# Performance work log

Measured on AMD Instinct MI355X. Metric: run time of the kernel, lower is better.

The kernel has to match this reference:

```python
import jax, jax.numpy as jnp
import numpy as np

N_IN = 1_000_000   # input mesh vertices
C = 128            # feature channels
N_OUT = 250_000


def setup_inputs() -> dict:
    key = jax.random.key(0)
    k1, k2, k3 = jax.random.split(key, 3)
    inputs = jax.random.normal(k1, (N_IN, C), dtype=jnp.float32)
    # cluster representative vertex for each input vertex
    vt_replace = jax.random.randint(k2, (N_IN,), 0, N_IN, dtype=jnp.int32)
    # output vertex id assigned to each (representative) vertex
    vt_map = jax.random.randint(k3, (N_IN,), 0, N_OUT, dtype=jnp.int32)
    return {"inputs": inputs, "vt_replace": vt_replace, "vt_map": vt_map, "vt_out": N_OUT}


def reference(inputs, vt_replace, vt_map, vt_out):
    # segment id of each input vertex: output slot of its cluster representative
    seg = vt_map[vt_replace]                     # [N_IN] int32 in [0, vt_out)
    # scatter-max reduce over irregular clusters -> [vt_out, C]
    out = jax.ops.segment_max(inputs, seg, num_segments=vt_out)
    # empty output vertices get 0 (segment_max fills with -inf)
    out = jnp.where(jnp.isfinite(out), out, jnp.zeros((), out.dtype))
    return out
```

## Files before the change

kernel.cpp:

```cpp
#include <hip/hip_runtime.h>
#include <stdint.h>

#define C_CH 128
#define SCAN_THREADS 256
#define SCAN_PER_THREAD 8
#define SCAN_ELEMS (SCAN_THREADS * SCAN_PER_THREAD)

typedef float floatx4 __attribute__((ext_vector_type(4)));

__device__ __forceinline__ unsigned fkey(float x) {
  unsigned b = __float_as_uint(x);
  return b ^ ((unsigned)((int)b >> 31) | 0x80000000u);
}
__device__ __forceinline__ float fdec(unsigned k) {
  unsigned b = (k & 0x80000000u) ? (k & 0x7FFFFFFFu) : ~k;
  return __uint_as_float(b);
}

__global__ __launch_bounds__(256) void pool_atomic(
    const float4* __restrict__ in4, const int* __restrict__ vt_replace,
    const int* __restrict__ vt_map, unsigned* __restrict__ outk, int64_t n4) {
  const int64_t stride = (int64_t)gridDim.x * blockDim.x;
  for (int64_t t = (int64_t)blockIdx.x * blockDim.x + threadIdx.x; t < n4;
       t += stride) {
    const int row = (int)(t >> 5);
    const int c4  = (int)(t & 31);
    int s = 0;
    if ((threadIdx.x & 31) == 0) s = vt_map[vt_replace[row]];
    s = __shfl(s, 0, 32);
    const float4 v = in4[t];
    unsigned* o = outk + ((int64_t)s << 7) + (c4 << 2);
    atomicMax(o + 0, fkey(v.x));
    atomicMax(o + 1, fkey(v.y));
    atomicMax(o + 2, fkey(v.z));
    atomicMax(o + 3, fkey(v.w));
  }
}
__global__ __launch_bounds__(256) void decode_k(unsigned* __restrict__ io, int64_t n4) {
  const int64_t stride = (int64_t)gridDim.x * blockDim.x;
  for (int64_t t = (int64_t)blockIdx.x * blockDim.x + threadIdx.x; t < n4;
       t += stride) {
    uint4* p = ((uint4*)io) + t;
    uint4 k = *p;
    float4 f;
    f.x = k.x ? fdec(k.x) : 0.0f;
    f.y = k.y ? fdec(k.y) : 0.0f;
    f.z = k.z ? fdec(k.z) : 0.0f;
    f.w = k.w ? fdec(k.w) : 0.0f;
    *(float4*)p = f;
  }
}


__global__ __launch_bounds__(256) void zero_u32(unsigned* __restrict__ p, int m) {
  const int stride = gridDim.x * blockDim.x;
  for (int i = blockIdx.x * blockDim.x + threadIdx.x; i < m; i += stride)
    p[i] = 0u;
}

__global__ __launch_bounds__(256) void seg_hist(
    const int* __restrict__ vt_replace, const int* __restrict__ vt_map,
    unsigned* __restrict__ counts, int n) {
  const int stride = gridDim.x * blockDim.x;
  for (int i = blockIdx.x * blockDim.x + threadIdx.x; i < n; i += stride) {
    const int s = vt_map[vt_replace[i]];
    atomicAdd(&counts[s], 1u);
  }
}

__global__ __launch_bounds__(SCAN_THREADS) void scan_reduce(
    const unsigned* __restrict__ counts, unsigned* __restrict__ bsums, int m) {
  __shared__ unsigned tot[SCAN_THREADS];
  const int base = blockIdx.x * SCAN_ELEMS + threadIdx.x * SCAN_PER_THREAD;
  unsigned s = 0;
  for (int j = 0; j < SCAN_PER_THREAD; ++j) {
    const int i = base + j;
    s += (i < m) ? counts[i] : 0u;
  }
  tot[threadIdx.x] = s;
  __syncthreads();
  for (int off = SCAN_THREADS / 2; off > 0; off >>= 1) {
    if (threadIdx.x < off) tot[threadIdx.x] += tot[threadIdx.x + off];
    __syncthreads();
  }
  if (threadIdx.x == 0) bsums[blockIdx.x] = tot[0];
}

__global__ void scan_bsums(unsigned* __restrict__ bsums, int g) {
  if (blockIdx.x == 0 && threadIdx.x == 0) {
    unsigned run = 0;
    for (int i = 0; i < g; ++i) { const unsigned t = bsums[i]; bsums[i] = run; run += t; }
  }
}

__global__ __launch_bounds__(SCAN_THREADS) void scan_down(
    const unsigned* __restrict__ counts, const unsigned* __restrict__ bsums,
    unsigned* __restrict__ cursor, int m) {
  __shared__ unsigned tot[SCAN_THREADS];
  const int base = blockIdx.x * SCAN_ELEMS + threadIdx.x * SCAN_PER_THREAD;
  unsigned v[SCAN_PER_THREAD];
  unsigned s = 0;
  for (int j = 0; j < SCAN_PER_THREAD; ++j) {
    const int i = base + j;
    v[j] = (i < m) ? counts[i] : 0u;
    s += v[j];
  }
  tot[threadIdx.x] = s;
  __syncthreads();
  for (int off = 1; off < SCAN_THREADS; off <<= 1) {
    unsigned t = (threadIdx.x >= (unsigned)off) ? tot[threadIdx.x - off] : 0u;
    __syncthreads();
    tot[threadIdx.x] += t;
    __syncthreads();
  }
  unsigned excl = (threadIdx.x ? tot[threadIdx.x - 1] : 0u) + bsums[blockIdx.x];
  for (int j = 0; j < SCAN_PER_THREAD; ++j) {
    const int i = base + j;
    if (i < m) cursor[i] = excl;
    excl += v[j];
  }
}

__global__ __launch_bounds__(256) void scatter_rows(
    const int* __restrict__ vt_replace, const int* __restrict__ vt_map,
    unsigned* __restrict__ cursor, int* __restrict__ rowids, int n) {
  const int stride = gridDim.x * blockDim.x;
  for (int i = blockIdx.x * blockDim.x + threadIdx.x; i < n; i += stride) {
    const int s = vt_map[vt_replace[i]];
    const unsigned p = atomicAdd(&cursor[s], 1u);
    rowids[p] = i;
  }
}

__device__ __forceinline__ floatx4 fmax4(floatx4 a, floatx4 b) {
  floatx4 r;
  r.x = fmaxf(a.x, b.x);
  r.y = fmaxf(a.y, b.y);
  r.z = fmaxf(a.z, b.z);
  r.w = fmaxf(a.w, b.w);
  return r;
}

__global__ __launch_bounds__(256) void gather_max4(
    const floatx4* __restrict__ in4, const int* __restrict__ rowids,
    const unsigned* __restrict__ cursor_end, const unsigned* __restrict__ counts,
    floatx4* __restrict__ out4, int m) {
  const int s = blockIdx.x * 8 + (threadIdx.x >> 5);
  if (s >= m) return;
  const int q = threadIdx.x & 31;
  const unsigned end = cursor_end[s];
  const unsigned cnt = counts[s];
  const unsigned start = end - cnt;

  floatx4 acc = (floatx4)(-INFINITY);

  for (unsigned base = start; base < end; base += 32) {
    const int nn = (int)min(32u, end - base);
    int rid = 0;
    if (q < nn) rid = rowids[base + q];
    int j = 0;
    for (; j + 4 <= nn; j += 4) {
      const int r0 = __shfl(rid, j + 0, 32);
      const int r1 = __shfl(rid, j + 1, 32);
      const int r2 = __shfl(rid, j + 2, 32);
      const int r3 = __shfl(rid, j + 3, 32);
      const floatx4 v0 = __builtin_nontemporal_load(&in4[(int64_t)r0 * 32 + q]);
      const floatx4 v1 = __builtin_nontemporal_load(&in4[(int64_t)r1 * 32 + q]);
      const floatx4 v2 = __builtin_nontemporal_load(&in4[(int64_t)r2 * 32 + q]);
      const floatx4 v3 = __builtin_nontemporal_load(&in4[(int64_t)r3 * 32 + q]);
      acc = fmax4(acc, fmax4(fmax4(v0, v1), fmax4(v2, v3)));
    }
    for (; j < nn; ++j) {
      const int r = __shfl(rid, j, 32);
      const floatx4 v = __builtin_nontemporal_load(&in4[(int64_t)r * 32 + q]);
      acc = fmax4(acc, v);
    }
  }
  if (cnt == 0) acc = (floatx4)(0.0f);
  __builtin_nontemporal_store(acc, &out4[(int64_t)s * 32 + q]);
}

extern "C" void kernel_launch(void* const* d_in, const int* in_sizes, int n_in_args,
                              void* d_out, int out_size, void* d_ws, size_t ws_size,
                              hipStream_t stream) {
  (void)n_in_args;
  const float*  in         = (const float*)d_in[0];
  const int*    vt_replace = (const int*)d_in[1];
  const int*    vt_map     = (const int*)d_in[2];
  const int     n_in = in_sizes[1];
  const int     m    = out_size / C_CH;

  uintptr_t p = (uintptr_t)d_ws;
  auto carve = [&](size_t bytes) {
    uintptr_t r = p;
    p += (bytes + 255) & ~(size_t)255;
    return (void*)r;
  };
  int*      rowids = (int*)carve((size_t)n_in * 4);
  unsigned* counts = (unsigned*)carve((size_t)m * 4);
  unsigned* cursor = (unsigned*)carve((size_t)m * 4);
  unsigned* bsums  = (unsigned*)carve(4096);
  const size_t needed = p - (uintptr_t)d_ws;

  if (ws_size < needed) {
    unsigned* outk = (unsigned*)d_out;
    (void)hipMemsetAsync(d_out, 0, (size_t)out_size * sizeof(float), stream);
    const int64_t n4 = (int64_t)n_in * (C_CH / 4);
    pool_atomic<<<2048, 256, 0, stream>>>((const float4*)in, vt_replace, vt_map, outk, n4);
    decode_k<<<2048, 256, 0, stream>>>(outk, (int64_t)out_size / 4);
    return;
  }

  zero_u32<<<256, 256, 0, stream>>>(counts, m);

  seg_hist<<<2048, 256, 0, stream>>>(vt_replace, vt_map, counts, n_in);

  const int g1 = (m + SCAN_ELEMS - 1) / SCAN_ELEMS;
  scan_reduce<<<g1, SCAN_THREADS, 0, stream>>>(counts, bsums, m);
  scan_bsums<<<1, 64, 0, stream>>>(bsums, g1);
  scan_down<<<g1, SCAN_THREADS, 0, stream>>>(counts, bsums, cursor, m);

  scatter_rows<<<2048, 256, 0, stream>>>(vt_replace, vt_map, cursor, rowids, n_in);

  const int gc = (m + 7) / 8;
  gather_max4<<<gc, 256, 0, stream>>>((const floatx4*)in, rowids, cursor, counts,
                                      (floatx4*)d_out, m);
}
```

Measured before the change: 235.3 us.

## Replace three-kernel prefix scan with atomic offset allocation per wavefront

```diff
diff --git a/kernel.cpp b/kernel.cpp
--- a/kernel.cpp
+++ b/kernel.cpp
@@ -2,9 +2,6 @@
 #include <stdint.h>
 
 #define C_CH 128
-#define SCAN_THREADS 256
-#define SCAN_PER_THREAD 8
-#define SCAN_ELEMS (SCAN_THREADS * SCAN_PER_THREAD)
 
 typedef float floatx4 __attribute__((ext_vector_type(4)));
 
@@ -68,57 +65,23 @@
   }
 }
 
-__global__ __launch_bounds__(SCAN_THREADS) void scan_reduce(
-    const unsigned* __restrict__ counts, unsigned* __restrict__ bsums, int m) {
-  __shared__ unsigned tot[SCAN_THREADS];
-  const int base = blockIdx.x * SCAN_ELEMS + threadIdx.x * SCAN_PER_THREAD;
-  unsigned s = 0;
-  for (int j = 0; j < SCAN_PER_THREAD; ++j) {
-    const int i = base + j;
-    s += (i < m) ? counts[i] : 0u;
+__global__ __launch_bounds__(256) void alloc_offsets(
+    const unsigned* __restrict__ counts, unsigned* __restrict__ cursor,
+    unsigned* __restrict__ total, int m) {
+  const int i = blockIdx.x * blockDim.x + threadIdx.x;
+  const int lane = threadIdx.x & 63;
+  const unsigned c = (i < m) ? counts[i] : 0u;
+  unsigned x = c;
+  for (int d = 1; d < 64; d <<= 1) {
+    const unsigned t = __shfl_up(x, d, 64);
+    if (lane >= d) x += t;
   }
-  tot[threadIdx.x] = s;
-  __syncthreads();
-  for (int off = SCAN_THREADS / 2; off > 0; off >>= 1) {
-    if (threadIdx.x < off) tot[threadIdx.x] += tot[threadIdx.x + off];
-    __syncthreads();
-  }
-  if (threadIdx.x == 0) bsums[blockIdx.x] = tot[0];
-}
-
-__global__ void scan_bsums(unsigned* __restrict__ bsums, int g) {
-  if (blockIdx.x == 0 && threadIdx.x == 0) {
-    unsigned run = 0;
-    for (int i = 0; i < g; ++i) { const unsigned t = bsums[i]; bsums[i] = run; run += t; }
-  }
-}
-
-__global__ __launch_bounds__(SCAN_THREADS) void scan_down(
-    const unsigned* __restrict__ counts, const unsigned* __restrict__ bsums,
-    unsigned* __restrict__ cursor, int m) {
-  __shared__ unsigned tot[SCAN_THREADS];
-  const int base = blockIdx.x * SCAN_ELEMS + threadIdx.x * SCAN_PER_THREAD;
-  unsigned v[SCAN_PER_THREAD];
-  unsigned s = 0;
-  for (int j = 0; j < SCAN_PER_THREAD; ++j) {
-    const int i = base + j;
-    v[j] = (i < m) ? counts[i] : 0u;
-    s += v[j];
-  }
-  tot[threadIdx.x] = s;
-  __syncthreads();
-  for (int off = 1; off < SCAN_THREADS; off <<= 1) {
-    unsigned t = (threadIdx.x >= (unsigned)off) ? tot[threadIdx.x - off] : 0u;
-    __syncthreads();
-    tot[threadIdx.x] += t;
-    __syncthreads();
-  }
-  unsigned excl = (threadIdx.x ? tot[threadIdx.x - 1] : 0u) + bsums[blockIdx.x];
-  for (int j = 0; j < SCAN_PER_THREAD; ++j) {
-    const int i = base + j;
-    if (i < m) cursor[i] = excl;
-    excl += v[j];
-  }
+  const unsigned excl = x - c;
+  const unsigned tot  = __shfl(x, 63, 64);
+  unsigned base = 0;
+  if (lane == 63) base = atomicAdd(total, tot);
+  base = __shfl(base, 63, 64);
+  if (i < m) cursor[i] = base + excl;
 }
 
 __global__ __launch_bounds__(256) void scatter_rows(
@@ -158,22 +121,17 @@
     const int nn = (int)min(32u, end - base);
     int rid = 0;
     if (q < nn) rid = rowids[base + q];
-    int j = 0;
-    for (; j + 4 <= nn; j += 4) {
-      const int r0 = __shfl(rid, j + 0, 32);
-      const int r1 = __shfl(rid, j + 1, 32);
-      const int r2 = __shfl(rid, j + 2, 32);
-      const int r3 = __shfl(rid, j + 3, 32);
+    const int last = nn - 1;
+    for (int j = 0; j < nn; j += 4) {
+      const int r0 = __shfl(rid, j, 32);
+      const int r1 = __shfl(rid, min(j + 1, last), 32);
+      const int r2 = __shfl(rid, min(j + 2, last), 32);
+      const int r3 = __shfl(rid, min(j + 3, last), 32);
       const floatx4 v0 = __builtin_nontemporal_load(&in4[(int64_t)r0 * 32 + q]);
       const floatx4 v1 = __builtin_nontemporal_load(&in4[(int64_t)r1 * 32 + q]);
       const floatx4 v2 = __builtin_nontemporal_load(&in4[(int64_t)r2 * 32 + q]);
       const floatx4 v3 = __builtin_nontemporal_load(&in4[(int64_t)r3 * 32 + q]);
       acc = fmax4(acc, fmax4(fmax4(v0, v1), fmax4(v2, v3)));
-    }
-    for (; j < nn; ++j) {
-      const int r = __shfl(rid, j, 32);
-      const floatx4 v = __builtin_nontemporal_load(&in4[(int64_t)r * 32 + q]);
-      acc = fmax4(acc, v);
     }
   }
   if (cnt == 0) acc = (floatx4)(0.0f);
@@ -197,9 +155,9 @@
     return (void*)r;
   };
   int*      rowids = (int*)carve((size_t)n_in * 4);
-  unsigned* counts = (unsigned*)carve((size_t)m * 4);
+  unsigned* counts = (unsigned*)carve(((size_t)m + 1) * 4);
   unsigned* cursor = (unsigned*)carve((size_t)m * 4);
-  unsigned* bsums  = (unsigned*)carve(4096);
+  unsigned* total  = counts + m;
   const size_t needed = p - (uintptr_t)d_ws;
 
   if (ws_size < needed) {
@@ -211,14 +169,11 @@
     return;
   }
 
-  zero_u32<<<256, 256, 0, stream>>>(counts, m);
+  zero_u32<<<256, 256, 0, stream>>>(counts, m + 1);
 
   seg_hist<<<2048, 256, 0, stream>>>(vt_replace, vt_map, counts, n_in);
 
-  const int g1 = (m + SCAN_ELEMS - 1) / SCAN_ELEMS;
-  scan_reduce<<<g1, SCAN_THREADS, 0, stream>>>(counts, bsums, m);
-  scan_bsums<<<1, 64, 0, stream>>>(bsums, g1);
-  scan_down<<<g1, SCAN_THREADS, 0, stream>>>(counts, bsums, cursor, m);
+  alloc_offsets<<<(m + 255) / 256, 256, 0, stream>>>(counts, cursor, total, m);
 
   scatter_rows<<<2048, 256, 0, stream>>>(vt_replace, vt_map, cursor, rowids, n_in);
 
```

Result: slower. 260.9 us (+10.9%).
